# Kernel tuning notes

Measured on AMD Instinct MI355X. Metric: run time of the kernel, lower is better.

Reference implementation:

```python
import math
import jax, jax.numpy as jnp
import numpy as np

D = 1024        # latent_dim
H = 16          # num latent heads
HD = D // H     # head dim = 64
T_EMB = 9       # max(diffusion_steps+1, 2)
CLIP = 1.0      # latent_update_clip
LN_EPS = 1e-5


def layer_norm(x, g, b):
    m = jnp.mean(x, axis=-1, keepdims=True)
    v = jnp.mean(jnp.square(x - m), axis=-1, keepdims=True)
    return (x - m) * jax.lax.rsqrt(v + LN_EPS) * g + b


def setup_inputs() -> dict:
    key = jax.random.key(0)
    ks = jax.random.split(key, 10)
    B, S = 64, 64
    s = 0.02
    return {
        "latents": jax.random.normal(ks[0], (B, S, D), jnp.float32),
        "t_table": jax.random.normal(ks[1], (T_EMB, D), jnp.float32) * s,
        "attn_g": jnp.ones((D,), jnp.float32),
        "attn_b": jnp.zeros((D,), jnp.float32),
        "ffn_g": jnp.ones((D,), jnp.float32),
        "ffn_b": jnp.zeros((D,), jnp.float32),
        "Wq": jax.random.normal(ks[2], (D, D), jnp.float32) * s,
        "Wk": jax.random.normal(ks[3], (D, D), jnp.float32) * s,
        "Wv": jax.random.normal(ks[4], (D, D), jnp.float32) * s,
        "Wo": jax.random.normal(ks[5], (D, D), jnp.float32) * s,
        "Win": jax.random.normal(ks[6], (2 * D, D), jnp.float32) * s,
        "b_in": jnp.zeros((2 * D,), jnp.float32),
        "Wout": jax.random.normal(ks[7], (D, 2 * D), jnp.float32) * s,
        "b_out": jnp.zeros((D,), jnp.float32),
        "steps": 8,
    }


def _slot_attention(x, Wq, Wk, Wv, Wo):
    B, S, _ = x.shape
    scale = 1.0 / math.sqrt(HD)
    # torch Linear: y = x @ W.T ; weights stored (out, in)
    q = (x @ Wq.T).reshape(B, S, H, HD)
    k = (x @ Wk.T).reshape(B, S, H, HD)
    v = (x @ Wv.T).reshape(B, S, H, HD)
    scores = jnp.einsum("bqhd,bkhd->bhqk", q, k) * scale
    probs = jax.nn.softmax(scores, axis=-1)
    out = jnp.einsum("bhqk,bkhd->bqhd", probs, v).reshape(B, S, D)
    return out @ Wo.T


def reference(latents, t_table, attn_g, attn_b, ffn_g, ffn_b,
              Wq, Wk, Wv, Wo, Win, b_in, Wout, b_out, steps):
    h = latents
    for step in range(steps):
        step_id = min(step, T_EMB - 1)
        t_emb = t_table[step_id][None, None, :]          # [1,1,D]
        attn_update = _slot_attention(layer_norm(h + t_emb, attn_g, attn_b),
                                      Wq, Wk, Wv, Wo)
        ffn_in = layer_norm(h + t_emb + attn_update, ffn_g, ffn_b)
        ffn_update = jax.nn.silu(ffn_in @ Win.T + b_in) @ Wout.T + b_out
        update = attn_update + ffn_update
        unorm = jnp.maximum(jnp.linalg.norm(update, axis=-1, keepdims=True), 1e-6)
        update = update * jnp.minimum(CLIP / unorm, 1.0)
        h = h + update / steps
    return h
```

## Files before the change

kernel.cpp:

```cpp
#include <hip/hip_runtime.h>
#include <hip/hip_bf16.h>

typedef __attribute__((ext_vector_type(8))) short bf16x8;
typedef __attribute__((ext_vector_type(4))) float f32x4;
typedef __attribute__((ext_vector_type(4))) int i32x4;

static __device__ __forceinline__ short f2bf(float f) {
    __hip_bfloat16 h = __float2bfloat16(f);
    return __builtin_bit_cast(short, h);
}
static __device__ __forceinline__ float bf2f(short s) {
    unsigned u = ((unsigned)(unsigned short)s) << 16;
    return __builtin_bit_cast(float, u);
}

static __device__ __forceinline__ void gload_lds16(const short* g, short* l) {
    __builtin_amdgcn_global_load_lds((const __attribute__((address_space(1))) void*)g,
                                     (__attribute__((address_space(3))) void*)l, 16, 0, 0);
}

__global__ void convert_all_kernel(
    const float* __restrict__ Wq, const float* __restrict__ Wk, const float* __restrict__ Wv,
    const float* __restrict__ Wo, const float* __restrict__ Win, const float* __restrict__ Wout,
    short* __restrict__ wQKV, short* __restrict__ wO, short* __restrict__ wIn, short* __restrict__ wOut)
{
    const int M1 = 1024 * 1024;
    for (int i = blockIdx.x * blockDim.x + threadIdx.x; i < 8 * M1; i += gridDim.x * blockDim.x) {
        if (i < 3 * M1) {
            float v = (i < M1) ? Wq[i] : (i < 2 * M1) ? Wk[i - M1] : Wv[i - 2 * M1];
            wQKV[i] = f2bf(v);
        } else if (i < 4 * M1) {
            wO[i - 3 * M1] = f2bf(Wo[i - 3 * M1]);
        } else if (i < 6 * M1) {
            wIn[i - 4 * M1] = f2bf(Win[i - 4 * M1]);
        } else {
            wOut[i - 6 * M1] = f2bf(Wout[i - 6 * M1]);
        }
    }
}

__global__ __launch_bounds__(256) void first_ln_kernel(
    const float* __restrict__ latents, float* __restrict__ h,
    const float* __restrict__ trow,
    const float* __restrict__ g, const float* __restrict__ bb,
    short* __restrict__ out)
{
    const int row = blockIdx.x;
    const int tid = threadIdx.x;
    const int lane = tid & 63;
    const int wid = tid >> 6;
    __shared__ float red[4];
    const float* hr = latents + (size_t)row * 1024;
    float x[4];
    float s = 0.f;
    #pragma unroll
    for (int i = 0; i < 4; ++i) {
        int c = tid + i * 256;
        float hv = hr[c];
        h[(size_t)row * 1024 + c] = hv;
        x[i] = hv + trow[c]; s += x[i];
    }
    #pragma unroll
    for (int o = 32; o >= 1; o >>= 1) s += __shfl_xor(s, o, 64);
    if (lane == 0) red[wid] = s;
    __syncthreads();
    float mean = (red[0] + red[1] + red[2] + red[3]) * (1.0f / 1024.0f);
    __syncthreads();
    float s2 = 0.f;
    #pragma unroll
    for (int i = 0; i < 4; ++i) { float d = x[i] - mean; s2 += d * d; }
    #pragma unroll
    for (int o = 32; o >= 1; o >>= 1) s2 += __shfl_xor(s2, o, 64);
    if (lane == 0) red[wid] = s2;
    __syncthreads();
    float var = (red[0] + red[1] + red[2] + red[3]) * (1.0f / 1024.0f);
    float rstd = rsqrtf(var + 1e-5f);
    #pragma unroll
    for (int i = 0; i < 4; ++i) {
        int c = tid + i * 256;
        out[(size_t)row * 1024 + c] = f2bf((x[i] - mean) * rstd * g[c] + bb[c]);
    }
}

__global__ __launch_bounds__(256) void ln_kernel(
    const float* __restrict__ hsrc, const float* __restrict__ trow,
    const short* __restrict__ add,
    const float* __restrict__ g, const float* __restrict__ bb,
    short* __restrict__ out)
{
    const int row = blockIdx.x;
    const int tid = threadIdx.x;
    const int lane = tid & 63;
    const int wid = tid >> 6;
    __shared__ float red[4];
    const float* hr = hsrc + (size_t)row * 1024;
    float x[4];
    float s = 0.f;
    #pragma unroll
    for (int i = 0; i < 4; ++i) {
        int c = tid + i * 256;
        float v = hr[c] + trow[c];
        if (add) v += bf2f(add[(size_t)row * 1024 + c]);
        x[i] = v; s += v;
    }
    #pragma unroll
    for (int o = 32; o >= 1; o >>= 1) s += __shfl_xor(s, o, 64);
    if (lane == 0) red[wid] = s;
    __syncthreads();
    float mean = (red[0] + red[1] + red[2] + red[3]) * (1.0f / 1024.0f);
    __syncthreads();
    float s2 = 0.f;
    #pragma unroll
    for (int i = 0; i < 4; ++i) { float d = x[i] - mean; s2 += d * d; }
    #pragma unroll
    for (int o = 32; o >= 1; o >>= 1) s2 += __shfl_xor(s2, o, 64);
    if (lane == 0) red[wid] = s2;
    __syncthreads();
    float var = (red[0] + red[1] + red[2] + red[3]) * (1.0f / 1024.0f);
    float rstd = rsqrtf(var + 1e-5f);
    #pragma unroll
    for (int i = 0; i < 4; ++i) {
        int c = tid + i * 256;
        out[(size_t)row * 1024 + c] = f2bf((x[i] - mean) * rstd * g[c] + bb[c]);
    }
}

__global__ __launch_bounds__(256) void clipln_kernel(
    const short* __restrict__ upd, float* __restrict__ h,
    const float* __restrict__ trow,
    const float* __restrict__ g, const float* __restrict__ bb,
    short* __restrict__ out)
{
    const int row = blockIdx.x;
    const int tid = threadIdx.x;
    const int lane = tid & 63;
    const int wid = tid >> 6;
    __shared__ float red[4];
    const short* ur = upd + (size_t)row * 1024;
    float u[4], hn[4];
    float s = 0.f;
    #pragma unroll
    for (int i = 0; i < 4; ++i) { u[i] = bf2f(ur[tid + i * 256]); s += u[i] * u[i]; }
    #pragma unroll
    for (int o = 32; o >= 1; o >>= 1) s += __shfl_xor(s, o, 64);
    if (lane == 0) red[wid] = s;
    __syncthreads();
    float nrm = sqrtf(red[0] + red[1] + red[2] + red[3]);
    float scale = fminf(1.0f / fmaxf(nrm, 1e-6f), 1.0f) * 0.125f;
    __syncthreads();
    float sm = 0.f;
    #pragma unroll
    for (int i = 0; i < 4; ++i) {
        int c = tid + i * 256;
        hn[i] = h[(size_t)row * 1024 + c] + u[i] * scale;
        h[(size_t)row * 1024 + c] = hn[i];
        hn[i] += trow[c];
        sm += hn[i];
    }
    #pragma unroll
    for (int o = 32; o >= 1; o >>= 1) sm += __shfl_xor(sm, o, 64);
    if (lane == 0) red[wid] = sm;
    __syncthreads();
    float mean = (red[0] + red[1] + red[2] + red[3]) * (1.0f / 1024.0f);
    __syncthreads();
    float s2 = 0.f;
    #pragma unroll
    for (int i = 0; i < 4; ++i) { float d = hn[i] - mean; s2 += d * d; }
    #pragma unroll
    for (int o = 32; o >= 1; o >>= 1) s2 += __shfl_xor(s2, o, 64);
    if (lane == 0) red[wid] = s2;
    __syncthreads();
    float var = (red[0] + red[1] + red[2] + red[3]) * (1.0f / 1024.0f);
    float rstd = rsqrtf(var + 1e-5f);
    #pragma unroll
    for (int i = 0; i < 4; ++i) {
        int c = tid + i * 256;
        out[(size_t)row * 1024 + c] = f2bf((hn[i] - mean) * rstd * g[c] + bb[c]);
    }
}

template<int BM, int BN, int NT, int ACT, int ADD, int BIAS>
__global__ __launch_bounds__(NT) void gemm_t(
    const short* __restrict__ A, const short* __restrict__ B,
    const float* __restrict__ bias, const short* __restrict__ addsrc,
    short* __restrict__ Cout, int M, int N, int K)
{
    const int nwg = gridDim.x * gridDim.y;
    const int orig = blockIdx.y * gridDim.x + blockIdx.x;
    const int swzid = (orig & 7) * (nwg >> 3) + (orig >> 3);
    const int bn = (swzid % gridDim.x) * BN;
    const int bm = (swzid / gridDim.x) * BM;

    __shared__ __align__(16) short As[2][BM * 64];
    __shared__ __align__(16) short Bs[2][BN * 64];
    const int tid = threadIdx.x;
    const int lane = tid & 63;
    const int wid = tid >> 6;
    const int l15 = lane & 15;
    const int l4 = lane >> 4;

    constexpr int WN = BN / 64;
    const int rowbase = (wid / WN) * 64;
    const int colbase = (wid % WN) * 64;

    constexpr int SA = BM * 8;
    constexpr int SB = BN * 8;
    constexpr int AIT = (SA + NT - 1) / NT;
    constexpr int BIT = SB / NT;
    constexpr int LW = SA / NT + SB / NT;

    f32x4 acc[4][4];
    #pragma unroll
    for (int m = 0; m < 4; ++m)
        #pragma unroll
        for (int n = 0; n < 4; ++n)
            acc[m][n] = (f32x4)(0.f);

    auto stage = [&](int k0, int buf) {
        #pragma unroll
        for (int i = 0; i < AIT; ++i) {
            int slot = i * NT + tid;
            if (AIT * NT == SA || slot < SA) {
                int row = slot >> 3;
                int colb = (slot & 7) * 16;
                int swz = (row & 7) << 4;
                const short* g = A + (size_t)(bm + row) * K + k0 + ((colb ^ swz) >> 1);
                gload_lds16(g, (short*)((char*)As[buf] + slot * 16));
            }
        }
        #pragma unroll
        for (int i = 0; i < BIT; ++i) {
            int slot = i * NT + tid;
            int row = slot >> 3;
            int colb = (slot & 7) * 16;
            int swz = (row & 7) << 4;
            const short* g = B + (size_t)(bn + row) * K + k0 + ((colb ^ swz) >> 1);
            gload_lds16(g, (short*)((char*)Bs[buf] + slot * 16));
        }
    };

    stage(0, 0);
    const int nt = K >> 6;
    for (int t = 0; t < nt; ++t) {
        const int cur = t & 1;
        if (t + 1 < nt) {
            stage((t + 1) << 6, cur ^ 1);
            if constexpr (LW == 5)      asm volatile("s_waitcnt vmcnt(5)" ::: "memory");
            else if constexpr (LW == 6) asm volatile("s_waitcnt vmcnt(6)" ::: "memory");
            else if constexpr (LW == 8) asm volatile("s_waitcnt vmcnt(8)" ::: "memory");
            else                        asm volatile("s_waitcnt vmcnt(4)" ::: "memory");
        } else {
            asm volatile("s_waitcnt vmcnt(0)" ::: "memory");
        }
        __builtin_amdgcn_s_barrier();
        #pragma unroll
        for (int ks = 0; ks < 2; ++ks) {
            int kb = ks * 64 + l4 * 16;
            bf16x8 a[4], b[4];
            #pragma unroll
            for (int m = 0; m < 4; ++m) {
                int row = rowbase + m * 16 + l15;
                a[m] = *(const bf16x8*)((const char*)As[cur] + row * 128 + (kb ^ ((row & 7) << 4)));
            }
            #pragma unroll
            for (int n = 0; n < 4; ++n) {
                int row = colbase + n * 16 + l15;
                b[n] = *(const bf16x8*)((const char*)Bs[cur] + row * 128 + (kb ^ ((row & 7) << 4)));
            }
            #pragma unroll
            for (int m = 0; m < 4; ++m)
                #pragma unroll
                for (int n = 0; n < 4; ++n)
                    acc[m][n] = __builtin_amdgcn_mfma_f32_16x16x32_bf16(a[m], b[n], acc[m][n], 0, 0, 0);
        }
        __builtin_amdgcn_s_barrier();
    }

    #pragma unroll
    for (int m = 0; m < 4; ++m) {
        int row = bm + rowbase + m * 16 + l4 * 4;
        #pragma unroll
        for (int n = 0; n < 4; ++n) {
            int col = bn + colbase + n * 16 + l15;
            float bv = BIAS ? bias[col] : 0.f;
            #pragma unroll
            for (int r = 0; r < 4; ++r) {
                float v = acc[m][n][r] + bv;
                if (ACT) v = v / (1.f + __expf(-v));
                if (ADD) v += bf2f(addsrc[(size_t)(row + r) * N + col]);
                Cout[(size_t)(row + r) * N + col] = f2bf(v);
            }
        }
    }
}

__global__ __launch_bounds__(256) void attn_kernel(
    const short* __restrict__ qkv,
    short* __restrict__ ctx)
{
    const int blk = blockIdx.x;
    const int b = blk >> 4, hh = blk & 15;
    const int bs0 = b * 64;
    __shared__ __align__(16) short qs[64 * 64];
    __shared__ __align__(16) short ks_[64 * 64];
    __shared__ __align__(16) short vt[64 * 64];
    __shared__ __align__(16) short ps[64 * 64];
    const int tid = threadIdx.x;
    const int lane = tid & 63;
    const int wid = tid >> 6;
    const int l15 = lane & 15;
    const int l4 = lane >> 4;

    #pragma unroll
    for (int i = 0; i < 2; ++i) {
        int slot = i * 256 + tid;
        int row = slot >> 3;
        int colb = (slot & 7) * 16;
        int swz = (row & 7) << 4;
        const short* gq = qkv + (size_t)(bs0 + row) * 3072 + hh * 64 + (slot & 7) * 8;
        *(i32x4*)((char*)qs + row * 128 + (colb ^ swz)) = *(const i32x4*)gq;
        const short* gk = qkv + (size_t)(bs0 + row) * 3072 + 1024 + hh * 64 + (slot & 7) * 8;
        *(i32x4*)((char*)ks_ + row * 128 + (colb ^ swz)) = *(const i32x4*)gk;
        const short* gv = qkv + (size_t)(bs0 + row) * 3072 + 2048 + hh * 64 + (slot & 7) * 8;
        i32x4 vv = *(const i32x4*)gv;
        const short* ve = (const short*)&vv;
        #pragma unroll
        for (int j = 0; j < 8; ++j) {
            int d = (slot & 7) * 8 + j;
            *(short*)((char*)vt + d * 128 + ((row * 2) ^ ((d & 7) << 4))) = ve[j];
        }
    }
    __syncthreads();

    f32x4 sc[4];
    #pragma unroll
    for (int n = 0; n < 4; ++n) sc[n] = (f32x4)(0.f);
    #pragma unroll
    for (int ksz = 0; ksz < 2; ++ksz) {
        int kb = ksz * 64 + l4 * 16;
        int arow = wid * 16 + l15;
        bf16x8 af = *(const bf16x8*)((const char*)qs + arow * 128 + (kb ^ ((arow & 7) << 4)));
        #pragma unroll
        for (int n = 0; n < 4; ++n) {
            int brow = n * 16 + l15;
            bf16x8 bf = *(const bf16x8*)((const char*)ks_ + brow * 128 + (kb ^ ((brow & 7) << 4)));
            sc[n] = __builtin_amdgcn_mfma_f32_16x16x32_bf16(af, bf, sc[n], 0, 0, 0);
        }
    }
    float sm[4];
    #pragma unroll
    for (int r = 0; r < 4; ++r) {
        float m = -1e30f;
        #pragma unroll
        for (int n = 0; n < 4; ++n) { sc[n][r] *= 0.125f; m = fmaxf(m, sc[n][r]); }
        #pragma unroll
        for (int o = 1; o < 16; o <<= 1) m = fmaxf(m, __shfl_xor(m, o, 64));
        float s = 0.f;
        #pragma unroll
        for (int n = 0; n < 4; ++n) { sc[n][r] = __expf(sc[n][r] - m); s += sc[n][r]; }
        #pragma unroll
        for (int o = 1; o < 16; o <<= 1) s += __shfl_xor(s, o, 64);
        sm[r] = 1.f / s;
    }
    #pragma unroll
    for (int n = 0; n < 4; ++n)
        #pragma unroll
        for (int r = 0; r < 4; ++r) {
            int row = wid * 16 + l4 * 4 + r;
            int col = n * 16 + l15;
            *(short*)((char*)ps + row * 128 + ((col * 2) ^ ((row & 7) << 4))) = f2bf(sc[n][r] * sm[r]);
        }
    __syncthreads();

    f32x4 o[4];
    #pragma unroll
    for (int n = 0; n < 4; ++n) o[n] = (f32x4)(0.f);
    #pragma unroll
    for (int ksz = 0; ksz < 2; ++ksz) {
        int kb = ksz * 64 + l4 * 16;
        int arow = wid * 16 + l15;
        bf16x8 af = *(const bf16x8*)((const char*)ps + arow * 128 + (kb ^ ((arow & 7) << 4)));
        #pragma unroll
        for (int n = 0; n < 4; ++n) {
            int vrow = n * 16 + l15;
            bf16x8 bf = *(const bf16x8*)((const char*)vt + vrow * 128 + (kb ^ ((vrow & 7) << 4)));
            o[n] = __builtin_amdgcn_mfma_f32_16x16x32_bf16(af, bf, o[n], 0, 0, 0);
        }
    }
    #pragma unroll
    for (int n = 0; n < 4; ++n)
        #pragma unroll
        for (int r = 0; r < 4; ++r) {
            int row = wid * 16 + l4 * 4 + r;
            int col = n * 16 + l15;
            ctx[(size_t)(bs0 + row) * 1024 + hh * 64 + col] = f2bf(o[n][r]);
        }
}

__global__ __launch_bounds__(256) void clip_kernel(const short* __restrict__ upd, float* __restrict__ h) {
    const int row = blockIdx.x;
    const int tid = threadIdx.x;
    const int lane = tid & 63;
    const int wid = tid >> 6;
    __shared__ float red[4];
    const short* ur = upd + (size_t)row * 1024;
    float x[4];
    float s = 0.f;
    #pragma unroll
    for (int i = 0; i < 4; ++i) { x[i] = bf2f(ur[tid + i * 256]); s += x[i] * x[i]; }
    #pragma unroll
    for (int o = 32; o >= 1; o >>= 1) s += __shfl_xor(s, o, 64);
    if (lane == 0) red[wid] = s;
    __syncthreads();
    float nrm = sqrtf(red[0] + red[1] + red[2] + red[3]);
    float unorm = fmaxf(nrm, 1e-6f);
    float scale = fminf(1.0f / unorm, 1.0f) * 0.125f;
    #pragma unroll
    for (int i = 0; i < 4; ++i) {
        int c = tid + i * 256;
        h[(size_t)row * 1024 + c] += x[i] * scale;
    }
}

extern "C" void kernel_launch(void* const* d_in, const int* in_sizes, int n_in,
                              void* d_out, int out_size, void* d_ws, size_t ws_size,
                              hipStream_t stream) {
    const float* latents = (const float*)d_in[0];
    const float* t_table = (const float*)d_in[1];
    const float* attn_g  = (const float*)d_in[2];
    const float* attn_b  = (const float*)d_in[3];
    const float* ffn_g   = (const float*)d_in[4];
    const float* ffn_b   = (const float*)d_in[5];
    const float* Wq      = (const float*)d_in[6];
    const float* Wk      = (const float*)d_in[7];
    const float* Wv      = (const float*)d_in[8];
    const float* Wo      = (const float*)d_in[9];
    const float* Win     = (const float*)d_in[10];
    const float* b_in    = (const float*)d_in[11];
    const float* Wout    = (const float*)d_in[12];
    const float* b_out   = (const float*)d_in[13];

    char* ws = (char*)d_ws;
    size_t off = 0;
    auto alloc = [&](size_t bytes) { char* p = ws + off; off += (bytes + 255) & ~(size_t)255; return p; };
    short* wQKV = (short*)alloc((size_t)3072 * 1024 * 2);
    short* wO   = (short*)alloc((size_t)1024 * 1024 * 2);
    short* wIn  = (short*)alloc((size_t)2048 * 1024 * 2);
    short* wOut = (short*)alloc((size_t)1024 * 2048 * 2);
    short* xln  = (short*)alloc((size_t)4096 * 1024 * 2);
    short* qkv  = (short*)alloc((size_t)4096 * 3072 * 2);
    short* hidden = qkv;
    short* ctx  = (short*)alloc((size_t)4096 * 1024 * 2);
    short* au   = (short*)alloc((size_t)4096 * 1024 * 2);
    short* upd  = (short*)alloc((size_t)4096 * 1024 * 2);

    float* h = (float*)d_out;

    convert_all_kernel<<<2048, 256, 0, stream>>>(Wq, Wk, Wv, Wo, Win, Wout, wQKV, wO, wIn, wOut);
    first_ln_kernel<<<4096, 256, 0, stream>>>(latents, h, t_table, attn_g, attn_b, xln);

    for (int step = 0; step < 8; ++step) {
        const float* trow = t_table + (size_t)step * 1024;
        gemm_t<128, 384, 768, 0, 0, 0><<<dim3(8, 32), 768, 0, stream>>>(xln, wQKV, nullptr, nullptr, qkv, 4096, 3072, 1024);
        attn_kernel<<<1024, 256, 0, stream>>>(qkv, ctx);
        gemm_t<128, 128, 256, 0, 0, 0><<<dim3(8, 32), 256, 0, stream>>>(ctx, wO, nullptr, nullptr, au, 4096, 1024, 1024);
        ln_kernel<<<4096, 256, 0, stream>>>(h, trow, au, ffn_g, ffn_b, xln);
        gemm_t<128, 256, 512, 1, 0, 1><<<dim3(8, 32), 512, 0, stream>>>(xln, wIn, b_in, nullptr, hidden, 4096, 2048, 1024);
        gemm_t<128, 128, 256, 0, 1, 1><<<dim3(8, 32), 256, 0, stream>>>(hidden, wOut, b_out, au, upd, 4096, 1024, 2048);
        if (step < 7) {
            clipln_kernel<<<4096, 256, 0, stream>>>(upd, h, t_table + (size_t)(step + 1) * 1024,
                                                    attn_g, attn_b, xln);
        } else {
            clip_kernel<<<4096, 256, 0, stream>>>(upd, h);
        }
    }
}
```

Before: 1.126 ms.

## Switch GEMMs to smaller 8-wave tiles with more blocks and restructured sync

All four GEMMs now use one 512-thread kernel with a fixed BN of 128 and BM of 128 or 64, so each wave owns a 32x64 or 32x32 output sub-tile instead of 64x64. The grids grow from 256 blocks to 512-768. The aim is to fill more of the CUs and to hide latency with more resident waves. The pipeline also moves the wait and barrier to the end of each iteration with a full vmcnt(0) drain. In exchange, operand reuse per wave drops, so each MFMA needs more LDS traffic, and the prefetch overlap becomes coarser.

```diff
diff --git a/kernel.cpp b/kernel.cpp
--- a/kernel.cpp
+++ b/kernel.cpp
@@ -179,8 +179,8 @@
     }
 }
 
-template<int BM, int BN, int NT, int ACT, int ADD, int BIAS>
-__global__ __launch_bounds__(NT) void gemm_t(
+template<int BM, int ACT, int ADD, int BIAS>
+__global__ __launch_bounds__(512) void gemm_kernel(
     const short* __restrict__ A, const short* __restrict__ B,
     const float* __restrict__ bias, const short* __restrict__ addsrc,
     short* __restrict__ Cout, int M, int N, int K)
@@ -188,49 +188,44 @@
     const int nwg = gridDim.x * gridDim.y;
     const int orig = blockIdx.y * gridDim.x + blockIdx.x;
     const int swzid = (orig & 7) * (nwg >> 3) + (orig >> 3);
-    const int bn = (swzid % gridDim.x) * BN;
+    const int bn = (swzid % gridDim.x) * 128;
     const int bm = (swzid / gridDim.x) * BM;
 
     __shared__ __align__(16) short As[2][BM * 64];
-    __shared__ __align__(16) short Bs[2][BN * 64];
+    __shared__ __align__(16) short Bs[2][128 * 64];
     const int tid = threadIdx.x;
     const int lane = tid & 63;
     const int wid = tid >> 6;
     const int l15 = lane & 15;
     const int l4 = lane >> 4;
 
-    constexpr int WN = BN / 64;
-    const int rowbase = (wid / WN) * 64;
-    const int colbase = (wid % WN) * 64;
-
-    constexpr int SA = BM * 8;
-    constexpr int SB = BN * 8;
-    constexpr int AIT = (SA + NT - 1) / NT;
-    constexpr int BIT = SB / NT;
-    constexpr int LW = SA / NT + SB / NT;
-
-    f32x4 acc[4][4];
-    #pragma unroll
-    for (int m = 0; m < 4; ++m)
-        #pragma unroll
-        for (int n = 0; n < 4; ++n)
+    constexpr int MF = 2;
+    constexpr int NF = (BM == 128) ? 4 : 2;
+    const int rowbase = (BM == 128) ? (wid >> 1) * 32 : (wid >> 2) * 32;
+    const int colbase = (BM == 128) ? (wid & 1) * 64 : (wid & 3) * 32;
+
+    constexpr int ALOADS = BM * 8 / 512;
+
+    f32x4 acc[MF][NF];
+    #pragma unroll
+    for (int m = 0; m < MF; ++m)
+        #pragma unroll
+        for (int n = 0; n < NF; ++n)
             acc[m][n] = (f32x4)(0.f);
 
     auto stage = [&](int k0, int buf) {
         #pragma unroll
-        for (int i = 0; i < AIT; ++i) {
-            int slot = i * NT + tid;
-            if (AIT * NT == SA || slot < SA) {
-                int row = slot >> 3;
-                int colb = (slot & 7) * 16;
-                int swz = (row & 7) << 4;
-                const short* g = A + (size_t)(bm + row) * K + k0 + ((colb ^ swz) >> 1);
-                gload_lds16(g, (short*)((char*)As[buf] + slot * 16));
-            }
-        }
-        #pragma unroll
-        for (int i = 0; i < BIT; ++i) {
-            int slot = i * NT + tid;
+        for (int i = 0; i < ALOADS; ++i) {
+            int slot = i * 512 + tid;
+            int row = slot >> 3;
+            int colb = (slot & 7) * 16;
+            int swz = (row & 7) << 4;
+            const short* g = A + (size_t)(bm + row) * K + k0 + ((colb ^ swz) >> 1);
+            gload_lds16(g, (short*)((char*)As[buf] + slot * 16));
+        }
+        #pragma unroll
+        for (int i = 0; i < 2; ++i) {
+            int slot = i * 512 + tid;
             int row = slot >> 3;
             int colb = (slot & 7) * 16;
             int swz = (row & 7) << 4;
@@ -240,47 +235,44 @@
     };
 
     stage(0, 0);
+    asm volatile("s_waitcnt vmcnt(0)" ::: "memory");
+    __builtin_amdgcn_s_barrier();
+
     const int nt = K >> 6;
     for (int t = 0; t < nt; ++t) {
         const int cur = t & 1;
-        if (t + 1 < nt) {
-            stage((t + 1) << 6, cur ^ 1);
-            if constexpr (LW == 5)      asm volatile("s_waitcnt vmcnt(5)" ::: "memory");
-            else if constexpr (LW == 6) asm volatile("s_waitcnt vmcnt(6)" ::: "memory");
-            else if constexpr (LW == 8) asm volatile("s_waitcnt vmcnt(8)" ::: "memory");
-            else                        asm volatile("s_waitcnt vmcnt(4)" ::: "memory");
-        } else {
-            asm volatile("s_waitcnt vmcnt(0)" ::: "memory");
-        }
-        __builtin_amdgcn_s_barrier();
+        if (t + 1 < nt) stage((t + 1) << 6, cur ^ 1);
         #pragma unroll
         for (int ks = 0; ks < 2; ++ks) {
             int kb = ks * 64 + l4 * 16;
-            bf16x8 a[4], b[4];
+            bf16x8 a[MF], b[NF];
             #pragma unroll
-            for (int m = 0; m < 4; ++m) {
+            for (int m = 0; m < MF; ++m) {
                 int row = rowbase + m * 16 + l15;
                 a[m] = *(const bf16x8*)((const char*)As[cur] + row * 128 + (kb ^ ((row & 7) << 4)));
             }
             #pragma unroll
-            for (int n = 0; n < 4; ++n) {
+            for (int n = 0; n < NF; ++n) {
                 int row = colbase + n * 16 + l15;
                 b[n] = *(const bf16x8*)((const char*)Bs[cur] + row * 128 + (kb ^ ((row & 7) << 4)));
             }
             #pragma unroll
-            for (int m = 0; m < 4; ++m)
+            for (int m = 0; m < MF; ++m)
                 #pragma unroll
-                for (int n = 0; n < 4; ++n)
+                for (int n = 0; n < NF; ++n)
                     acc[m][n] = __builtin_amdgcn_mfma_f32_16x16x32_bf16(a[m], b[n], acc[m][n], 0, 0, 0);
         }
-        __builtin_amdgcn_s_barrier();
-    }
-
-    #pragma unroll
-    for (int m = 0; m < 4; ++m) {
+        if (t + 1 < nt) {
+            asm volatile("s_waitcnt vmcnt(0)" ::: "memory");
+            __builtin_amdgcn_s_barrier();
+        }
+    }
+
+    #pragma unroll
+    for (int m = 0; m < MF; ++m) {
         int row = bm + rowbase + m * 16 + l4 * 4;
         #pragma unroll
-        for (int n = 0; n < 4; ++n) {
+        for (int n = 0; n < NF; ++n) {
             int col = bn + colbase + n * 16 + l15;
             float bv = BIAS ? bias[col] : 0.f;
             #pragma unroll
@@ -461,12 +453,12 @@
 
     for (int step = 0; step < 8; ++step) {
         const float* trow = t_table + (size_t)step * 1024;
-        gemm_t<128, 384, 768, 0, 0, 0><<<dim3(8, 32), 768, 0, stream>>>(xln, wQKV, nullptr, nullptr, qkv, 4096, 3072, 1024);
+        gemm_kernel<128, 0, 0, 0><<<dim3(24, 32), 512, 0, stream>>>(xln, wQKV, nullptr, nullptr, qkv, 4096, 3072, 1024);
         attn_kernel<<<1024, 256, 0, stream>>>(qkv, ctx);
-        gemm_t<128, 128, 256, 0, 0, 0><<<dim3(8, 32), 256, 0, stream>>>(ctx, wO, nullptr, nullptr, au, 4096, 1024, 1024);
+        gemm_kernel<64, 0, 0, 0><<<dim3(8, 64), 512, 0, stream>>>(ctx, wO, nullptr, nullptr, au, 4096, 1024, 1024);
         ln_kernel<<<4096, 256, 0, stream>>>(h, trow, au, ffn_g, ffn_b, xln);
-        gemm_t<128, 256, 512, 1, 0, 1><<<dim3(8, 32), 512, 0, stream>>>(xln, wIn, b_in, nullptr, hidden, 4096, 2048, 1024);
-        gemm_t<128, 128, 256, 0, 1, 1><<<dim3(8, 32), 256, 0, stream>>>(hidden, wOut, b_out, au, upd, 4096, 1024, 2048);
+        gemm_kernel<128, 1, 0, 1><<<dim3(16, 32), 512, 0, stream>>>(xln, wIn, b_in, nullptr, hidden, 4096, 2048, 1024);
+        gemm_kernel<64, 0, 1, 1><<<dim3(8, 64), 512, 0, stream>>>(hidden, wOut, b_out, au, upd, 4096, 1024, 2048);
         if (step < 7) {
             clipln_kernel<<<4096, 256, 0, stream>>>(upd, h, t_table + (size_t)(step + 1) * 1024,
                                                     attn_g, attn_b, xln);
```

After: 1.062 ms. 5.6% less time.
